# Optimization experiments

Hardware: AMD Instinct MI355X
Metric: run time of the kernel (lower is better)

Reference implementation:

```python
import jax, jax.numpy as jnp
import numpy as np


def setup_inputs() -> dict:
    key = jax.random.key(0)
    ks = jax.random.split(key, 8)
    N, F, H, B = 500_000, 128, 64, 1024
    x1 = jax.random.normal(ks[0], (N, F), dtype=jnp.float32)
    x2 = jax.random.normal(ks[1], (N, F), dtype=jnp.float32)
    batch1 = jax.random.randint(ks[2], (N,), 0, B, dtype=jnp.int32)
    batch2 = jax.random.randint(ks[3], (N,), 0, B, dtype=jnp.int32)
    # attn_mlp params: Linear(F->H), tanh, Linear(H->1)
    W1 = jax.random.normal(ks[4], (F, H), dtype=jnp.float32) * (1.0 / np.sqrt(F))
    b1 = jnp.zeros((H,), dtype=jnp.float32)
    W2 = jax.random.normal(ks[5], (H, 1), dtype=jnp.float32) * (1.0 / np.sqrt(H))
    b2 = jnp.zeros((1,), dtype=jnp.float32)
    return dict(x1=x1, x2=x2, batch1=batch1, batch2=batch2, B=B,
                W1=W1, b1=b1, W2=W2, b2=b2)


def _attn_pool(x, batch, B, W1, b1, W2, b2):
    # score = attn_mlp(x).squeeze(-1)  : [N]
    score = (jnp.tanh(x @ W1 + b1) @ W2 + b2)[:, 0]
    # per-graph (segment) softmax, numerically stable
    m = jax.ops.segment_max(score, batch, num_segments=B)      # [B]
    e = jnp.exp(score - m[batch])                               # [N]
    s = jax.ops.segment_sum(e, batch, num_segments=B)           # [B]
    attn = e / s[batch]                                         # [N]
    # dropout is identity in eval mode
    # scatter-sum pooling of attn-weighted features
    return jax.ops.segment_sum(attn[:, None] * x, batch, num_segments=B)  # [B, F]


def reference(x1, x2, batch1, batch2, B, W1, b1, W2, b2):
    p1 = _attn_pool(x1, batch1, B, W1, b1, W2, b2)
    p2 = _attn_pool(x2, batch2, B, W1, b1, W2, b2)
    # mean over node types (stack(...).mean(0))
    return 0.5 * (p1 + p2)
```

## Files before the change

kernel.cpp:

```cpp
#include <hip/hip_runtime.h>
#include <hip/hip_bf16.h>
#include <math.h>

#define NF 128
#define NH 64
#define NB 1024
#define CAP 768
#define SPAD 16
#define LDSW 136

struct NodeW { int idx; float w; };

typedef __attribute__((ext_vector_type(8))) short short8;
typedef __attribute__((ext_vector_type(4))) float f32x4;

static __device__ inline short f2bf(float f) {
    __hip_bfloat16 h = __float2bfloat16(f);
    short r; __builtin_memcpy(&r, &h, 2); return r;
}

static __device__ inline float tanh_fast(float a) {
    float t = __expf(-2.0f * fabsf(a));
    float th = __fdividef(1.0f - t, 1.0f + t);
    return copysignf(th, a);
}

__global__ __launch_bounds__(256) void mtap_prep(
    const float* __restrict__ W1, const float* __restrict__ W2,
    const float* __restrict__ bias2, unsigned short* __restrict__ w1t,
    float* __restrict__ mconst)
{
    int tid = threadIdx.x;
    #pragma unroll
    for (int i = 0; i < 32; ++i) {
        int L = tid + i * 256;
        int n = L >> 7, k = L & 127;
        w1t[L] = (unsigned short)f2bf(W1[k * NH + n]);
    }
    if (tid < 64) {
        float v = fabsf(W2[tid]);
        #pragma unroll
        for (int off = 32; off >= 1; off >>= 1) v += __shfl_down(v, off);
        if (tid == 0) mconst[0] = v + fabsf(bias2[0]);
    }
}

__global__ __launch_bounds__(256) void mtap_init(float* __restrict__ s,
                                                 int* __restrict__ cursor) {
    int i = blockIdx.x * 256 + threadIdx.x;
    if (i < 2 * NB * SPAD) { s[i] = 0.0f; cursor[i] = 0; }
}

__global__ __launch_bounds__(256, 2) void mtap_score(
    const float* __restrict__ x1, const float* __restrict__ x2,
    const int* __restrict__ g1, const int* __restrict__ g2,
    const unsigned short* __restrict__ w1t, const float* __restrict__ bias1,
    const float* __restrict__ W2, const float* __restrict__ bias2,
    const float* __restrict__ mconst,
    int* __restrict__ cursor, NodeW* __restrict__ bins,
    float* __restrict__ s_arr, int N)
{
    __shared__ unsigned short w1lds[64 * LDSW];
    int tid = threadIdx.x;

    #pragma unroll
    for (int i = 0; i < 4; ++i) {
        int lin = tid * 4 + i;
        int n = lin >> 4, c16 = lin & 15;
        short8 v = *(const short8*)(w1t + lin * 8);
        *(short8*)&w1lds[n * LDSW + c16 * 8] = v;
    }
    __syncthreads();

    int lane = tid & 63, w = tid >> 6;
    int c = lane & 15, q = lane >> 4;

    short8 bfrag[4][4];
    #pragma unroll
    for (int t = 0; t < 4; ++t)
        #pragma unroll
        for (int s = 0; s < 4; ++s)
            bfrag[t][s] = *(const short8*)&w1lds[(t * 16 + c) * LDSW + s * 32 + q * 8];

    float b1v[4], w2v[4];
    #pragma unroll
    for (int t = 0; t < 4; ++t) {
        b1v[t] = bias1[t * 16 + c];
        w2v[t] = W2[t * 16 + c];
    }
    float shift = bias2[0] - mconst[0];

    long twoN = 2L * N;
    int gw = blockIdx.x * 4 + w;
    long step = (long)gridDim.x * 4 * 32;

    for (long base = (long)gw * 32; base < twoN; base += step) {
        const float* rp[2];
        #pragma unroll
        for (int a = 0; a < 2; ++a) {
            long r = base + a * 16 + c;
            if (r >= twoN) r = twoN - 1;
            rp[a] = (r >= N) ? (x2 + (r - N) * NF) : (x1 + r * NF);
        }

        f32x4 acc[2][4];
        #pragma unroll
        for (int t = 0; t < 4; ++t)
            #pragma unroll
            for (int a = 0; a < 2; ++a)
                acc[a][t] = f32x4{b1v[t], b1v[t], b1v[t], b1v[t]};

        #pragma unroll
        for (int s = 0; s < 4; ++s) {
            short8 af[2];
            #pragma unroll
            for (int a = 0; a < 2; ++a) {
                const float4* p = (const float4*)(rp[a] + s * 32 + q * 8);
                float4 f0 = p[0], f1 = p[1];
                af[a] = short8{f2bf(f0.x), f2bf(f0.y), f2bf(f0.z), f2bf(f0.w),
                               f2bf(f1.x), f2bf(f1.y), f2bf(f1.z), f2bf(f1.w)};
            }
            #pragma unroll
            for (int t = 0; t < 4; ++t) {
                acc[0][t] = __builtin_amdgcn_mfma_f32_16x16x32_bf16(af[0], bfrag[t][s], acc[0][t], 0, 0, 0);
                acc[1][t] = __builtin_amdgcn_mfma_f32_16x16x32_bf16(af[1], bfrag[t][s], acc[1][t], 0, 0, 0);
            }
        }

        float p2[8];
        #pragma unroll
        for (int a = 0; a < 2; ++a)
            #pragma unroll
            for (int r = 0; r < 4; ++r) {
                float p = 0.0f;
                #pragma unroll
                for (int t = 0; t < 4; ++t)
                    p = fmaf(tanh_fast(acc[a][t][r]), w2v[t], p);
                p2[a * 4 + r] = p;
            }
        #pragma unroll
        for (int m = 1; m <= 8; m <<= 1)
            #pragma unroll
            for (int k = 0; k < 8; ++k)
                p2[k] += __shfl_xor(p2[k], m);

        if (c < 8) {
            float sv = p2[0];
            #pragma unroll
            for (int k = 1; k < 8; ++k) sv = (c == k) ? p2[k] : sv;
            int a = c >> 2, r = c & 3;
            long gid = base + a * 16 + q * 4 + r;
            if (gid < twoN) {
                int ty = gid >= N;
                int n = ty ? (int)(gid - N) : (int)gid;
                int seg = (ty ? g2 : g1)[n];
                int bin = ty * NB + seg;
                float e = __expf(sv + shift);
                int pos = atomicAdd(&cursor[bin * SPAD], 1);
                if (pos < CAP) bins[(long)bin * CAP + pos] = NodeW{n, e};
                atomicAdd(&s_arr[bin * SPAD], e);
            }
        }
    }
}

__global__ __launch_bounds__(256) void mtap_accum(
    const float* __restrict__ x1, const float* __restrict__ x2,
    const NodeW* __restrict__ bins, const int* __restrict__ cursor,
    const float* __restrict__ s_arr, float* __restrict__ out)
{
    int seg = blockIdx.x;
    int wv = threadIdx.x >> 6;
    int lane = threadIdx.x & 63;
    float ox = 0.0f, oy = 0.0f;

    #pragma unroll
    for (int ty = 0; ty < 2; ++ty) {
        int bin = ty * NB + seg;
        const float* x = ty ? x2 : x1;
        int cnt = min(cursor[bin * SPAD], CAP);
        float ssum = s_arr[bin * SPAD];
        float scale = (cnt > 0) ? 0.5f / ssum : 0.0f;
        const NodeW* b = bins + (long)bin * CAP;
        float ax = 0.0f, ay = 0.0f;
        int j = wv;
        for (; j + 28 < cnt; j += 32) {
            NodeW pp[8];
            float2 vv[8];
            #pragma unroll
            for (int u = 0; u < 8; ++u) pp[u] = b[j + 4 * u];
            #pragma unroll
            for (int u = 0; u < 8; ++u)
                vv[u] = *(const float2*)(x + (long)pp[u].idx * NF + 2 * lane);
            #pragma unroll
            for (int u = 0; u < 8; ++u) {
                ax = fmaf(pp[u].w, vv[u].x, ax);
                ay = fmaf(pp[u].w, vv[u].y, ay);
            }
        }
        for (; j < cnt; j += 4) {
            NodeW p = b[j];
            float2 v = *(const float2*)(x + (long)p.idx * NF + 2 * lane);
            ax = fmaf(p.w, v.x, ax);
            ay = fmaf(p.w, v.y, ay);
        }
        ox = fmaf(scale, ax, ox);
        oy = fmaf(scale, ay, oy);
    }

    __shared__ float red[4][NF];
    *(float2*)&red[wv][2 * lane] = make_float2(ox, oy);
    __syncthreads();
    int t = threadIdx.x;
    if (t < NF)
        out[seg * NF + t] = red[0][t] + red[1][t] + red[2][t] + red[3][t];
}

extern "C" void kernel_launch(void* const* d_in, const int* in_sizes, int n_in,
                              void* d_out, int out_size, void* d_ws, size_t ws_size,
                              hipStream_t stream)
{
    const float* x1    = (const float*)d_in[0];
    const float* x2    = (const float*)d_in[1];
    const int*   g1    = (const int*)d_in[2];
    const int*   g2    = (const int*)d_in[3];
    const float* W1    = (const float*)d_in[5];
    const float* bias1 = (const float*)d_in[6];
    const float* W2    = (const float*)d_in[7];
    const float* bias2 = (const float*)d_in[8];
    int N = in_sizes[2];

    char* wsp = (char*)d_ws;
    NodeW* bins = (NodeW*)wsp;                 wsp += (size_t)2 * NB * CAP * sizeof(NodeW);
    float* s_arr = (float*)wsp;                wsp += (size_t)2 * NB * SPAD * sizeof(float);
    int* cursor = (int*)wsp;                   wsp += (size_t)2 * NB * SPAD * sizeof(int);
    unsigned short* w1t = (unsigned short*)wsp; wsp += (size_t)NF * NH * sizeof(unsigned short);
    float* mconst = (float*)wsp;
    float* out = (float*)d_out;

    hipLaunchKernelGGL(mtap_prep, dim3(1), dim3(256), 0, stream,
                       W1, W2, bias2, w1t, mconst);
    hipLaunchKernelGGL(mtap_init, dim3((2 * NB * SPAD + 255) / 256), dim3(256), 0,
                       stream, s_arr, cursor);
    hipLaunchKernelGGL(mtap_score, dim3(1024), dim3(256), 0, stream,
                       x1, x2, g1, g2, w1t, bias1, W2, bias2, mconst,
                       cursor, bins, s_arr, N);
    hipLaunchKernelGGL(mtap_accum, dim3(NB), dim3(256), 0, stream,
                       x1, x2, bins, cursor, s_arr, out);
}
```

Measured before the change: 654.5 us.

## Raise score-kernel occupancy by streaming W1 fragments from LDS and hoisting cursor atomics

The W1 B-fragments are no longer held in registers (64 VGPRs). They are reloaded from LDS on each MFMA step, which lets launch bounds rise from 2 to 6 blocks per SIMD and the grid grow from 1024 to 1536 blocks. The batch-index load and cursor atomicAdd move to the top of each tile so their latency overlaps the x loads and MFMAs. tanh is rewritten as a clamped exp2-based formula. The cost is extra LDS reads per MFMA, and the higher occupancy target may cause register spills.

```diff
diff --git a/kernel.cpp b/kernel.cpp
--- a/kernel.cpp
+++ b/kernel.cpp
@@ -20,9 +20,9 @@
 }
 
 static __device__ inline float tanh_fast(float a) {
-    float t = __expf(-2.0f * fabsf(a));
-    float th = __fdividef(1.0f - t, 1.0f + t);
-    return copysignf(th, a);
+    float ac = fminf(fmaxf(a, -15.0f), 15.0f);
+    float t = exp2f(ac * 2.8853900817779268f);
+    return __fdividef(t - 1.0f, t + 1.0f);
 }
 
 __global__ __launch_bounds__(256) void mtap_prep(
@@ -51,7 +51,7 @@
     if (i < 2 * NB * SPAD) { s[i] = 0.0f; cursor[i] = 0; }
 }
 
-__global__ __launch_bounds__(256, 2) void mtap_score(
+__global__ __launch_bounds__(256, 6) void mtap_score(
     const float* __restrict__ x1, const float* __restrict__ x2,
     const int* __restrict__ g1, const int* __restrict__ g2,
     const unsigned short* __restrict__ w1t, const float* __restrict__ bias1,
@@ -75,13 +75,6 @@
     int lane = tid & 63, w = tid >> 6;
     int c = lane & 15, q = lane >> 4;
 
-    short8 bfrag[4][4];
-    #pragma unroll
-    for (int t = 0; t < 4; ++t)
-        #pragma unroll
-        for (int s = 0; s < 4; ++s)
-            bfrag[t][s] = *(const short8*)&w1lds[(t * 16 + c) * LDSW + s * 32 + q * 8];
-
     float b1v[4], w2v[4];
     #pragma unroll
     for (int t = 0; t < 4; ++t) {
@@ -95,6 +88,20 @@
     long step = (long)gridDim.x * 4 * 32;
 
     for (long base = (long)gw * 32; base < twoN; base += step) {
+        int pos = 0, bin = 0, nidx = 0, valid = 0;
+        if (c < 8) {
+            int a = c >> 2, r = c & 3;
+            long gid = base + a * 16 + q * 4 + r;
+            if (gid < twoN) {
+                valid = 1;
+                int ty = gid >= N;
+                nidx = ty ? (int)(gid - N) : (int)gid;
+                int seg = (ty ? g2 : g1)[nidx];
+                bin = ty * NB + seg;
+                pos = atomicAdd(&cursor[bin * SPAD], 1);
+            }
+        }
+
         const float* rp[2];
         #pragma unroll
         for (int a = 0; a < 2; ++a) {
@@ -122,8 +129,9 @@
             }
             #pragma unroll
             for (int t = 0; t < 4; ++t) {
-                acc[0][t] = __builtin_amdgcn_mfma_f32_16x16x32_bf16(af[0], bfrag[t][s], acc[0][t], 0, 0, 0);
-                acc[1][t] = __builtin_amdgcn_mfma_f32_16x16x32_bf16(af[1], bfrag[t][s], acc[1][t], 0, 0, 0);
+                short8 bf8 = *(const short8*)&w1lds[(t * 16 + c) * LDSW + s * 32 + q * 8];
+                acc[0][t] = __builtin_amdgcn_mfma_f32_16x16x32_bf16(af[0], bf8, acc[0][t], 0, 0, 0);
+                acc[1][t] = __builtin_amdgcn_mfma_f32_16x16x32_bf16(af[1], bf8, acc[1][t], 0, 0, 0);
             }
         }
 
@@ -144,22 +152,13 @@
             for (int k = 0; k < 8; ++k)
                 p2[k] += __shfl_xor(p2[k], m);
 
-        if (c < 8) {
+        if (valid) {
             float sv = p2[0];
             #pragma unroll
             for (int k = 1; k < 8; ++k) sv = (c == k) ? p2[k] : sv;
-            int a = c >> 2, r = c & 3;
-            long gid = base + a * 16 + q * 4 + r;
-            if (gid < twoN) {
-                int ty = gid >= N;
-                int n = ty ? (int)(gid - N) : (int)gid;
-                int seg = (ty ? g2 : g1)[n];
-                int bin = ty * NB + seg;
-                float e = __expf(sv + shift);
-                int pos = atomicAdd(&cursor[bin * SPAD], 1);
-                if (pos < CAP) bins[(long)bin * CAP + pos] = NodeW{n, e};
-                atomicAdd(&s_arr[bin * SPAD], e);
-            }
+            float e = __expf(sv + shift);
+            if (pos < CAP) bins[(long)bin * CAP + pos] = NodeW{nidx, e};
+            atomicAdd(&s_arr[bin * SPAD], e);
         }
     }
 }
@@ -242,7 +241,7 @@
                        W1, W2, bias2, w1t, mconst);
     hipLaunchKernelGGL(mtap_init, dim3((2 * NB * SPAD + 255) / 256), dim3(256), 0,
                        stream, s_arr, cursor);
-    hipLaunchKernelGGL(mtap_score, dim3(1024), dim3(256), 0, stream,
+    hipLaunchKernelGGL(mtap_score, dim3(1536), dim3(256), 0, stream,
                        x1, x2, g1, g2, w1t, bias1, W2, bias2, mconst,
                        cursor, bins, s_arr, N);
     hipLaunchKernelGGL(mtap_accum, dim3(NB), dim3(256), 0, stream,
```

Result: slower. 820.2 us (+25.3%).
